# Kernel optimization log

Hardware: AMD Instinct MI355X
Metric: run time of the kernel (lower is better)

Reference implementation:

```python
import jax, jax.numpy as jnp
import numpy as np

B, D_IN, H, C = 8192, 256, 512, 10
EXPANSION = 2
INTER = int(H * EXPANSION * 2 / 3)  # 682, matches torch int(dim*expansion*2/3)
K_OUTER, H_CYCLES, L_CYCLES = 4, 2, 3
EPS = 1e-6


def rms_norm(x):
    return x * jax.lax.rsqrt(jnp.mean(x * x, axis=-1, keepdims=True) + EPS)


def swiglu(x, Wgu, Wd):
    gate, up = jnp.split(x @ Wgu, 2, axis=-1)
    return (jax.nn.silu(gate) * up) @ Wd


def setup_inputs() -> dict:
    key = jax.random.key(0)
    ks = jax.random.split(key, 13)
    s = 0.02
    return {
        "x": jax.random.normal(ks[0], (B, D_IN), jnp.float32),
        "W_in": jax.random.normal(ks[1], (D_IN, H), jnp.float32) * s,
        "b_in": jnp.zeros((H,), jnp.float32),
        "W_fb": jax.random.normal(ks[2], (C, H), jnp.float32) * s,
        "b_fb": jnp.zeros((H,), jnp.float32),
        "Wgu1": jax.random.normal(ks[3], (H, 2 * INTER), jnp.float32) * s,
        "Wd1": jax.random.normal(ks[4], (INTER, H), jnp.float32) * s,
        "Wgu2": jax.random.normal(ks[5], (H, 2 * INTER), jnp.float32) * s,
        "Wd2": jax.random.normal(ks[6], (INTER, H), jnp.float32) * s,
        "H_init": jax.random.normal(ks[7], (H,), jnp.float32) * s,
        "L_init": jax.random.normal(ks[8], (H,), jnp.float32) * s,
        "W_out": jax.random.normal(ks[9], (H, C), jnp.float32) * s,
        "b_out": jnp.zeros((C,), jnp.float32),
    }


def reference(x, W_in, b_in, W_fb, b_fb, Wgu1, Wd1, Wgu2, Wd2,
              H_init, L_init, W_out, b_out):
    def block(h):  # TRMBlock: two post-norm SwiGLU sublayers
        h = rms_norm(h + swiglu(h, Wgu1, Wd1))
        h = rms_norm(h + swiglu(h, Wgu2, Wd2))
        return h

    def level(hidden, injection):  # TRMLevel with n_layers=1
        return block(hidden + injection)

    x_proj = x @ W_in + b_in                       # [B,H]
    z_H = jnp.broadcast_to(H_init, (x.shape[0], H))
    z_L = jnp.broadcast_to(L_init, (x.shape[0], H))
    feedback = jnp.zeros((x.shape[0], H), x.dtype)
    all_logits = []
    for k in range(K_OUTER):
        combined = x_proj + feedback
        for _h in range(H_CYCLES):
            for _l in range(L_CYCLES):
                z_L = level(z_L, z_H + combined)
            z_H = level(z_H, z_L)
        if k < K_OUTER - 1:  # grad_last_only=True: no_grad + detach
            z_H = jax.lax.stop_gradient(z_H)
            z_L = jax.lax.stop_gradient(z_L)
        logits = z_H @ W_out + b_out               # [B,C]
        all_logits.append(logits)
        probs = jax.nn.softmax(jax.lax.stop_gradient(logits), axis=-1)
        feedback = probs @ W_fb + b_fb
    return logits, jnp.stack(all_logits)
```

## Files before the change

kernel.cpp:

```cpp
#include <hip/hip_runtime.h>

#define DEVI __device__ __forceinline__

typedef __attribute__((ext_vector_type(8)))  short short8;
typedef __attribute__((ext_vector_type(4)))  short short4v;
typedef __attribute__((ext_vector_type(16))) float f32x16;

constexpr int NROW = 8192;
constexpr int HD   = 512;
constexpr int DIN  = 256;
constexpr int NC   = 10;

constexpr int NP  = 22;
constexpr int KT1 = 32;
constexpr int KT2 = 44;
constexpr int KTX = 16;
constexpr int NTH = 16;

constexpr int KSTEP1 = NP*64*32;
constexpr int KSTEPD = NTH*64*16;

constexpr int SZ_P1  = (KT1+4)*KSTEP1;
constexpr int SZ_PD  = (KT2+4)*KSTEPD;
constexpr int SZ_PIN = (KTX+4)*KSTEPD;

DEVI short f2bf(float x){
  unsigned u = __builtin_bit_cast(unsigned, x);
  unsigned r = u + 0x7FFFu + ((u >> 16) & 1u);
  return (short)(r >> 16);
}
DEVI float bf2f(short s){
  unsigned u = ((unsigned)(unsigned short)s) << 16;
  return __builtin_bit_cast(float, u);
}
DEVI f32x16 MF(short8 a, short8 b, f32x16 c){
  return __builtin_amdgcn_mfma_f32_32x32x16_bf16(a, b, c, 0, 0, 0);
}
DEVI f32x16 fzero(){
  f32x16 v;
  #pragma unroll
  for (int i = 0; i < 16; ++i) v[i] = 0.f;
  return v;
}

DEVI void silu_store(int p, const f32x16& cg, const f32x16& cu,
                     short* INh_, short* INl_, int l)
{
  const int m = l & 31, g = l >> 5;
  #pragma unroll
  for (int q = 0; q < 4; ++q) {
    short4v hi, lo;
    #pragma unroll
    for (int pos = 0; pos < 4; ++pos) {
      const int r = q*4 + pos;
      float gv = cg[r], uv = cu[r];
      float sv = (gv / (1.0f + __expf(-gv))) * uv;
      short h = f2bf(sv);
      hi[pos] = h;
      lo[pos] = f2bf(sv - bf2f(h));
    }
    const int kt2  = 2*p + (q >> 1);
    const int slot = ((q & 1) << 5) + m;
    const int base = (kt2*64 + slot)*8 + (g << 2);
    *(short4v*)&INh_[base] = hi;
    *(short4v*)&INl_[base] = lo;
  }
}

DEVI void g1_pair(const short* __restrict__ bW,
                  const short* __restrict__ A1h_, const short* __restrict__ A1l_,
                  int l, f32x16& ag, f32x16& au)
{
  short8 R0[4], R1[4];
  auto LD = [&](short8* R, int kt) {
    const short* p = bW + (size_t)kt*KSTEP1;
    R[0] = *(const short8*)(p);
    R[1] = *(const short8*)(p + 8);
    R[2] = *(const short8*)(p + 16);
    R[3] = *(const short8*)(p + 24);
  };
  LD(R0, 0); LD(R1, 1);
  #pragma unroll 1
  for (int kt = 0; kt < KT1; kt += 2) {
    #define G1STEP(R, u) { \
      short8 bh = *(const short8*)&A1h_[((kt+u)*64 + l)*8]; \
      short8 bl = *(const short8*)&A1l_[((kt+u)*64 + l)*8]; \
      ag = MF(R[0], bh, ag); ag = MF(R[1], bh, ag); ag = MF(R[0], bl, ag); \
      au = MF(R[2], bh, au); au = MF(R[3], bh, au); au = MF(R[2], bl, au); \
      LD(R, kt + u + 2); }
    G1STEP(R0, 0) G1STEP(R1, 1)
    #undef G1STEP
  }
}

template<int KT>
DEVI void g2_run(const short* __restrict__ bD,
                 const short* __restrict__ Bh_, const short* __restrict__ Bl_,
                 int l, f32x16& c0, f32x16& c1)
{
  short8 R0[4], R1[4];
  auto LD = [&](short8* R, int kt) {
    const short* p = bD + (size_t)kt*KSTEPD;
    R[0] = *(const short8*)(p);
    R[1] = *(const short8*)(p + 8);
    R[2] = *(const short8*)(p + 1024);
    R[3] = *(const short8*)(p + 1032);
  };
  LD(R0, 0); LD(R1, 1);
  #pragma unroll 1
  for (int kt = 0; kt < KT; kt += 2) {
    #define G2STEP(R, u) { \
      short8 bh = *(const short8*)&Bh_[((kt+u)*64 + l)*8]; \
      short8 bl = *(const short8*)&Bl_[((kt+u)*64 + l)*8]; \
      c0 = MF(R[0], bh, c0); c0 = MF(R[1], bh, c0); c0 = MF(R[0], bl, c0); \
      c1 = MF(R[2], bh, c1); c1 = MF(R[3], bh, c1); c1 = MF(R[2], bl, c1); \
      LD(R, kt + u + 2); }
    G2STEP(R0, 0) G2STEP(R1, 1)
    #undef G2STEP
  }
}

DEVI void sublayer(float (&S)[32], const short* __restrict__ PW, const short* __restrict__ PD,
                   short* A1h_, short* A1l_, short* INh_, short* INl_,
                   float* rmsS_, int w, int l)
{
  const int m = l & 31, g = l >> 5;
  #pragma unroll
  for (int t = 0; t < 2; ++t) {
    #pragma unroll
    for (int q = 0; q < 4; ++q) {
      short4v hi, lo;
      #pragma unroll
      for (int pos = 0; pos < 4; ++pos) {
        float v = S[t*16 + q*4 + pos];
        short h = f2bf(v);
        hi[pos] = h;
        lo[pos] = f2bf(v - bf2f(h));
      }
      const int kt   = 4*w + 2*t + (q >> 1);
      const int slot = ((q & 1) << 5) + m;
      const int base = (kt*64 + slot)*8 + (g << 2);
      *(short4v*)&A1h_[base] = hi;
      *(short4v*)&A1l_[base] = lo;
    }
  }
  __syncthreads();
  {
    f32x16 ag = fzero(), au = fzero();
    g1_pair(PW + ((size_t)(w*64 + l))*32, A1h_, A1l_, l, ag, au);
    silu_store(w, ag, au, INh_, INl_, l);
  }
  {
    f32x16 ag = fzero(), au = fzero();
    g1_pair(PW + ((size_t)((w + 8)*64 + l))*32, A1h_, A1l_, l, ag, au);
    silu_store(w + 8, ag, au, INh_, INl_, l);
  }
  if (w < 6) {
    f32x16 ag = fzero(), au = fzero();
    g1_pair(PW + ((size_t)((w + 16)*64 + l))*32, A1h_, A1l_, l, ag, au);
    silu_store(w + 16, ag, au, INh_, INl_, l);
  }
  __syncthreads();
  f32x16 c0 = fzero(), c1 = fzero();
  g2_run<KT2>(PD + ((size_t)(2*w*64 + l))*16, INh_, INl_, l, c0, c1);
  float ss = 0.f;
  #pragma unroll
  for (int s = 0; s < 32; ++s) {
    float y = S[s] + (s < 16 ? c0[s & 15] : c1[s & 15]);
    S[s] = y;
    ss += y*y;
  }
  ss += __shfl_xor(ss, 32);
  if (l < 32) rmsS_[w*32 + l] = ss;
  __syncthreads();
  float tot = 0.f;
  #pragma unroll
  for (int wv = 0; wv < 8; ++wv) tot += rmsS_[wv*32 + m];
  const float rinv = 1.0f / sqrtf(tot * (1.0f/512.0f) + 1e-6f);
  #pragma unroll
  for (int s = 0; s < 32; ++s) S[s] *= rinv;
}

__global__
__attribute__((amdgpu_flat_work_group_size(512, 512)))
__attribute__((amdgpu_waves_per_eu(2, 2)))
void trm_main(
    const float* __restrict__ x,
    const float* __restrict__ b_in,
    const float* __restrict__ W_fb,
    const float* __restrict__ b_fb,
    const float* __restrict__ H_init,
    const float* __restrict__ L_init,
    const float* __restrict__ W_out,
    const float* __restrict__ b_out,
    float* __restrict__ xp,
    const short* __restrict__ PIN,
    const short* __restrict__ P1, const short* __restrict__ PD1,
    const short* __restrict__ P2, const short* __restrict__ PD2,
    float* __restrict__ out)
{
  __shared__ alignas(16) char smem[156672];
  short* A1h  = (short*)(smem);
  short* A1l  = (short*)(smem + 32768);
  short* INh  = (short*)(smem + 65536);
  short* INl  = (short*)(smem + 110592);
  float* rmsS = (float*)(smem + 155648);
  float* lgS  = (float*)(smem);
  float* pbS  = (float*)(smem + 10240);

  const int tid = threadIdx.x;
  const int l = tid & 63;
  const int w = tid >> 6;
  const int m = l & 31;
  const int g = l >> 5;
  const int wg = blockIdx.x;
  const int row0 = wg * 32;

  float zL[32], zH[32], cb[32];

  #pragma unroll
  for (int kk = 0; kk < 2; ++kk) {
    const int kt = 2*w + kk;
    const float4* xr = (const float4*)(x + (size_t)(row0 + m)*DIN + kt*16 + g*8);
    float4 v0 = xr[0];
    float4 v1 = xr[1];
    float v[8] = {v0.x, v0.y, v0.z, v0.w, v1.x, v1.y, v1.z, v1.w};
    short8 hi, lo;
    #pragma unroll
    for (int i = 0; i < 8; ++i) {
      short h = f2bf(v[i]);
      hi[i] = h;
      lo[i] = f2bf(v[i] - bf2f(h));
    }
    const int base = (kt*64 + l)*8;
    *(short8*)&A1h[base] = hi;
    *(short8*)&A1l[base] = lo;
  }
  __syncthreads();
  {
    f32x16 c0 = fzero(), c1 = fzero();
    g2_run<KTX>(PIN + ((size_t)(2*w*64 + l))*16, A1h, A1l, l, c0, c1);
    #pragma unroll
    for (int s = 0; s < 32; ++s) {
      const int r = s & 15;
      const int cc = w*64 + (s >> 4)*32 + (r & 3) + ((r >> 2) << 3) + (g << 2);
      float v = (s < 16 ? c0[r] : c1[r]) + b_in[cc];
      cb[s] = v;
      xp[(size_t)(wg*8 + w)*2048 + s*64 + l] = v;
      zH[s] = H_init[cc];
      zL[s] = L_init[cc];
    }
  }
  __syncthreads();

  #pragma unroll 1
  for (int k = 0; k < 4; ++k) {
    #pragma unroll 1
    for (int hc = 0; hc < 2; ++hc) {
      #pragma unroll 1
      for (int li = 0; li < 3; ++li) {
        #pragma unroll
        for (int s = 0; s < 32; ++s) zL[s] += zH[s] + cb[s];
        sublayer(zL, P1, PD1, A1h, A1l, INh, INl, rmsS, w, l);
        sublayer(zL, P2, PD2, A1h, A1l, INh, INl, rmsS, w, l);
      }
      #pragma unroll
      for (int s = 0; s < 32; ++s) zH[s] += zL[s];
      sublayer(zH, P1, PD1, A1h, A1l, INh, INl, rmsS, w, l);
      sublayer(zH, P2, PD2, A1h, A1l, INh, INl, rmsS, w, l);
    }
    {
      float part[10];
      #pragma unroll
      for (int c = 0; c < NC; ++c) part[c] = 0.f;
      #pragma unroll
      for (int s = 0; s < 32; ++s) {
        const int r = s & 15;
        const int cc = w*64 + (s >> 4)*32 + (r & 3) + ((r >> 2) << 3) + (g << 2);
        const float zz = zH[s];
        #pragma unroll
        for (int c = 0; c < NC; ++c) part[c] += zz * W_out[cc*NC + c];
      }
      #pragma unroll
      for (int c = 0; c < NC; ++c) part[c] += __shfl_xor(part[c], 32);
      if (l < 32) {
        #pragma unroll
        for (int c = 0; c < NC; ++c) lgS[(w*32 + l)*NC + c] = part[c];
      }
      __syncthreads();
      if (w == 0 && l < 32) {
        float lg[10];
        #pragma unroll
        for (int c = 0; c < NC; ++c) lg[c] = b_out[c];
        #pragma unroll
        for (int wv = 0; wv < 8; ++wv) {
          #pragma unroll
          for (int c = 0; c < NC; ++c) lg[c] += lgS[(wv*32 + l)*NC + c];
        }
        const int row = row0 + l;
        #pragma unroll
        for (int c = 0; c < NC; ++c) out[(size_t)(1 + k)*81920 + row*NC + c] = lg[c];
        if (k == 3) {
          #pragma unroll
          for (int c = 0; c < NC; ++c) out[row*NC + c] = lg[c];
        }
        float mx = lg[0];
        #pragma unroll
        for (int c = 1; c < NC; ++c) mx = fmaxf(mx, lg[c]);
        float e[10], sum = 0.f;
        #pragma unroll
        for (int c = 0; c < NC; ++c) { e[c] = __expf(lg[c] - mx); sum += e[c]; }
        const float inv = 1.0f / sum;
        #pragma unroll
        for (int c = 0; c < NC; ++c) pbS[l*NC + c] = e[c] * inv;
      }
      __syncthreads();
      if (k < 3) {
        #pragma unroll
        for (int s = 0; s < 32; ++s) {
          const int r = s & 15;
          const int cc = w*64 + (s >> 4)*32 + (r & 3) + ((r >> 2) << 3) + (g << 2);
          float fb = b_fb[cc];
          #pragma unroll
          for (int c = 0; c < NC; ++c) fb += pbS[m*NC + c] * W_fb[c*HD + cc];
          cb[s] = xp[(size_t)(wg*8 + w)*2048 + s*64 + l] + fb;
        }
      }
      __syncthreads();
    }
  }
}

__global__ void prep_gu(const float* __restrict__ Wgu, short* __restrict__ P)
{
  const int t = blockIdx.x*256 + threadIdx.x;
  if (t >= KT1*NP*64) return;
  const int l = t & 63;
  const int rest = t >> 6;
  const int nt = rest % NP;
  const int kt = rest / NP;
  const int n  = nt*32 + (l & 31);
  const int kb = kt*16 + (l >> 5)*8;
  short8 gh8, gl8, uh8, ul8;
  #pragma unroll
  for (int i = 0; i < 8; ++i) {
    float gv = 0.f, uv = 0.f;
    if (n < 682) {
      gv = Wgu[(size_t)(kb + i)*1364 + n];
      uv = Wgu[(size_t)(kb + i)*1364 + 682 + n];
    }
    short gh = f2bf(gv); gh8[i] = gh; gl8[i] = f2bf(gv - bf2f(gh));
    short uh = f2bf(uv); uh8[i] = uh; ul8[i] = f2bf(uv - bf2f(uh));
  }
  short* dst = P + ((size_t)(kt*NP + nt)*64 + l)*32;
  *(short8*)(dst)      = gh8;
  *(short8*)(dst + 8)  = gl8;
  *(short8*)(dst + 16) = uh8;
  *(short8*)(dst + 24) = ul8;
}

__global__ void prep_d(const float* __restrict__ Wd, short* __restrict__ P)
{
  const int t = blockIdx.x*256 + threadIdx.x;
  if (t >= KT2*NTH*64) return;
  const int l = t & 63;
  const int rest = t >> 6;
  const int nt = rest % NTH;
  const int kt2 = rest / NTH;
  const int n  = nt*32 + (l & 31);
  const int kb = kt2*16 + (l >> 5)*8;
  short8 h8, l8;
  #pragma unroll
  for (int i = 0; i < 8; ++i) {
    const int k2 = kb + i;
    float v = (k2 < 682) ? Wd[(size_t)k2*HD + n] : 0.f;
    short h = f2bf(v); h8[i] = h; l8[i] = f2bf(v - bf2f(h));
  }
  short* dst = P + ((size_t)(kt2*NTH + nt)*64 + l)*16;
  *(short8*)(dst)     = h8;
  *(short8*)(dst + 8) = l8;
}

__global__ void prep_in(const float* __restrict__ Win, short* __restrict__ P)
{
  const int t = blockIdx.x*256 + threadIdx.x;
  if (t >= KTX*NTH*64) return;
  const int l = t & 63;
  const int rest = t >> 6;
  const int nt = rest % NTH;
  const int kt = rest / NTH;
  const int n  = nt*32 + (l & 31);
  const int kb = kt*16 + (l >> 5)*8;
  short8 h8, l8;
  #pragma unroll
  for (int i = 0; i < 8; ++i) {
    float v = Win[(size_t)(kb + i)*HD + n];
    short h = f2bf(v); h8[i] = h; l8[i] = f2bf(v - bf2f(h));
  }
  short* dst = P + ((size_t)(kt*NTH + nt)*64 + l)*16;
  *(short8*)(dst)     = h8;
  *(short8*)(dst + 8) = l8;
}

extern "C" void kernel_launch(void* const* d_in, const int* in_sizes, int n_in,
                              void* d_out, int out_size, void* d_ws, size_t ws_size,
                              hipStream_t stream)
{
  const float* x     = (const float*)d_in[0];
  const float* W_in  = (const float*)d_in[1];
  const float* b_in  = (const float*)d_in[2];
  const float* W_fb  = (const float*)d_in[3];
  const float* b_fb  = (const float*)d_in[4];
  const float* Wgu1  = (const float*)d_in[5];
  const float* Wd1   = (const float*)d_in[6];
  const float* Wgu2  = (const float*)d_in[7];
  const float* Wd2   = (const float*)d_in[8];
  const float* Hini  = (const float*)d_in[9];
  const float* Lini  = (const float*)d_in[10];
  const float* W_out = (const float*)d_in[11];
  const float* b_out = (const float*)d_in[12];
  float* out = (float*)d_out;

  char* ws = (char*)d_ws;
  size_t off = 0;
  auto alloc = [&](size_t bytes) {
    char* p = ws + off;
    off = (off + bytes + 255) & ~(size_t)255;
    return p;
  };
  float* xp  = (float*)alloc((size_t)NROW*HD*4);
  short* PIN = (short*)alloc((size_t)SZ_PIN*2);
  short* P1  = (short*)alloc((size_t)SZ_P1*2);
  short* PD1 = (short*)alloc((size_t)SZ_PD*2);
  short* P2  = (short*)alloc((size_t)SZ_P1*2);
  short* PD2 = (short*)alloc((size_t)SZ_PD*2);

  const int n1 = KT1*NP*64;
  prep_gu<<<(n1+255)/256, 256, 0, stream>>>(Wgu1, P1);
  prep_gu<<<(n1+255)/256, 256, 0, stream>>>(Wgu2, P2);
  const int n2 = KT2*NTH*64;
  prep_d<<<(n2+255)/256, 256, 0, stream>>>(Wd1, PD1);
  prep_d<<<(n2+255)/256, 256, 0, stream>>>(Wd2, PD2);
  const int n3 = KTX*NTH*64;
  prep_in<<<(n3+255)/256, 256, 0, stream>>>(W_in, PIN);

  trm_main<<<256, 512, 0, stream>>>(x, b_in, W_fb, b_fb, Hini, Lini, W_out, b_out,
      xp, PIN, P1, PD1, P2, PD2, out);
}
```

Baseline: 4.937 ms.

## Spill combined injection to global and reload residual from LDS split-bf16

Moves the per-thread combined injection array (cb) out of registers into a global buffer reloaded with float4 reads inside each injecting sublayer. The injection add is fused into the bf16 hi/lo split, and the residual is rebuilt from the LDS hi+lo copy instead of being kept live in registers. The aim is to cut register pressure at two waves per EU and avoid spills. The cost is extra global traffic per sublayer. The residual is also rebuilt from a bf16x2 split rather than exact fp32, which may change precision slightly.

```diff
diff --git a/kernel.cpp b/kernel.cpp
--- a/kernel.cpp
+++ b/kernel.cpp
@@ -120,11 +120,22 @@
   }
 }
 
-DEVI void sublayer(float (&S)[32], const short* __restrict__ PW, const short* __restrict__ PD,
+template<int INJ>
+DEVI void sublayer(float (&S)[32], const float (&O)[32], const float* __restrict__ cbRow,
+                   const short* __restrict__ PW, const short* __restrict__ PD,
                    short* A1h_, short* A1l_, short* INh_, short* INl_,
                    float* rmsS_, int w, int l)
 {
   const int m = l & 31, g = l >> 5;
+  float inj[32];
+  if (INJ == 1) {
+    const float4* cbp = (const float4*)cbRow;
+    #pragma unroll
+    for (int i = 0; i < 8; ++i) {
+      float4 t4 = cbp[i];
+      inj[4*i+0] = t4.x; inj[4*i+1] = t4.y; inj[4*i+2] = t4.z; inj[4*i+3] = t4.w;
+    }
+  }
   #pragma unroll
   for (int t = 0; t < 2; ++t) {
     #pragma unroll
@@ -132,7 +143,10 @@
       short4v hi, lo;
       #pragma unroll
       for (int pos = 0; pos < 4; ++pos) {
-        float v = S[t*16 + q*4 + pos];
+        const int s = t*16 + q*4 + pos;
+        float v = S[s];
+        if (INJ == 1) v += O[s] + inj[s];
+        if (INJ == 2) v += O[s];
         short h = f2bf(v);
         hi[pos] = h;
         lo[pos] = f2bf(v - bf2f(h));
@@ -165,10 +179,23 @@
   g2_run<KT2>(PD + ((size_t)(2*w*64 + l))*16, INh_, INl_, l, c0, c1);
   float ss = 0.f;
   #pragma unroll
-  for (int s = 0; s < 32; ++s) {
-    float y = S[s] + (s < 16 ? c0[s & 15] : c1[s & 15]);
-    S[s] = y;
-    ss += y*y;
+  for (int t = 0; t < 2; ++t) {
+    #pragma unroll
+    for (int q = 0; q < 4; ++q) {
+      const int kt   = 4*w + 2*t + (q >> 1);
+      const int slot = ((q & 1) << 5) + m;
+      const int base = (kt*64 + slot)*8 + (g << 2);
+      short4v hi = *(const short4v*)&A1h_[base];
+      short4v lo = *(const short4v*)&A1l_[base];
+      #pragma unroll
+      for (int pos = 0; pos < 4; ++pos) {
+        const int s = t*16 + q*4 + pos;
+        float h0 = bf2f(hi[pos]) + bf2f(lo[pos]);
+        float y = h0 + (s < 16 ? c0[s & 15] : c1[s & 15]);
+        S[s] = y;
+        ss += y*y;
+      }
+    }
   }
   ss += __shfl_xor(ss, 32);
   if (l < 32) rmsS_[w*32 + l] = ss;
@@ -194,6 +221,7 @@
     const float* __restrict__ W_out,
     const float* __restrict__ b_out,
     float* __restrict__ xp,
+    float* __restrict__ cbG,
     const short* __restrict__ PIN,
     const short* __restrict__ P1, const short* __restrict__ PD1,
     const short* __restrict__ P2, const short* __restrict__ PD2,
@@ -216,7 +244,9 @@
   const int wg = blockIdx.x;
   const int row0 = wg * 32;
 
-  float zL[32], zH[32], cb[32];
+  float zL[32], zH[32];
+  const size_t rowbase = (size_t)(wg*8 + w)*2048 + l*32;
+  const float* cbRow = cbG + rowbase;
 
   #pragma unroll
   for (int kk = 0; kk < 2; ++kk) {
@@ -240,15 +270,23 @@
   {
     f32x16 c0 = fzero(), c1 = fzero();
     g2_run<KTX>(PIN + ((size_t)(2*w*64 + l))*16, A1h, A1l, l, c0, c1);
+    float vals[32];
     #pragma unroll
     for (int s = 0; s < 32; ++s) {
       const int r = s & 15;
       const int cc = w*64 + (s >> 4)*32 + (r & 3) + ((r >> 2) << 3) + (g << 2);
       float v = (s < 16 ? c0[r] : c1[r]) + b_in[cc];
-      cb[s] = v;
-      xp[(size_t)(wg*8 + w)*2048 + s*64 + l] = v;
+      vals[s] = v;
       zH[s] = H_init[cc];
       zL[s] = L_init[cc];
+    }
+    float4* xpw = (float4*)(xp + rowbase);
+    float4* cbw = (float4*)(cbG + rowbase);
+    #pragma unroll
+    for (int i = 0; i < 8; ++i) {
+      float4 t4 = { vals[4*i+0], vals[4*i+1], vals[4*i+2], vals[4*i+3] };
+      xpw[i] = t4;
+      cbw[i] = t4;
     }
   }
   __syncthreads();
@@ -259,15 +297,11 @@
     for (int hc = 0; hc < 2; ++hc) {
       #pragma unroll 1
       for (int li = 0; li < 3; ++li) {
-        #pragma unroll
-        for (int s = 0; s < 32; ++s) zL[s] += zH[s] + cb[s];
-        sublayer(zL, P1, PD1, A1h, A1l, INh, INl, rmsS, w, l);
-        sublayer(zL, P2, PD2, A1h, A1l, INh, INl, rmsS, w, l);
-      }
-      #pragma unroll
-      for (int s = 0; s < 32; ++s) zH[s] += zL[s];
-      sublayer(zH, P1, PD1, A1h, A1l, INh, INl, rmsS, w, l);
-      sublayer(zH, P2, PD2, A1h, A1l, INh, INl, rmsS, w, l);
+        sublayer<1>(zL, zH, cbRow, P1, PD1, A1h, A1l, INh, INl, rmsS, w, l);
+        sublayer<0>(zL, zH, cbRow, P2, PD2, A1h, A1l, INh, INl, rmsS, w, l);
+      }
+      sublayer<2>(zH, zL, cbRow, P1, PD1, A1h, A1l, INh, INl, rmsS, w, l);
+      sublayer<0>(zH, zL, cbRow, P2, PD2, A1h, A1l, INh, INl, rmsS, w, l);
     }
     {
       float part[10];
@@ -316,14 +350,33 @@
       }
       __syncthreads();
       if (k < 3) {
+        float pb[10];
+        #pragma unroll
+        for (int c = 0; c < NC; ++c) pb[c] = pbS[m*NC + c];
+        float xa[32];
+        {
+          const float4* xpr = (const float4*)(xp + rowbase);
+          #pragma unroll
+          for (int i = 0; i < 8; ++i) {
+            float4 t4 = xpr[i];
+            xa[4*i+0] = t4.x; xa[4*i+1] = t4.y; xa[4*i+2] = t4.z; xa[4*i+3] = t4.w;
+          }
+        }
+        float cbv[32];
         #pragma unroll
         for (int s = 0; s < 32; ++s) {
           const int r = s & 15;
           const int cc = w*64 + (s >> 4)*32 + (r & 3) + ((r >> 2) << 3) + (g << 2);
           float fb = b_fb[cc];
           #pragma unroll
-          for (int c = 0; c < NC; ++c) fb += pbS[m*NC + c] * W_fb[c*HD + cc];
-          cb[s] = xp[(size_t)(wg*8 + w)*2048 + s*64 + l] + fb;
+          for (int c = 0; c < NC; ++c) fb += pb[c] * W_fb[c*HD + cc];
+          cbv[s] = xa[s] + fb;
+        }
+        float4* cbw = (float4*)(cbG + rowbase);
+        #pragma unroll
+        for (int i = 0; i < 8; ++i) {
+          float4 t4 = { cbv[4*i+0], cbv[4*i+1], cbv[4*i+2], cbv[4*i+3] };
+          cbw[i] = t4;
         }
       }
       __syncthreads();
@@ -429,6 +482,7 @@
     return p;
   };
   float* xp  = (float*)alloc((size_t)NROW*HD*4);
+  float* cbG = (float*)alloc((size_t)NROW*HD*4);
   short* PIN = (short*)alloc((size_t)SZ_PIN*2);
   short* P1  = (short*)alloc((size_t)SZ_P1*2);
   short* PD1 = (short*)alloc((size_t)SZ_PD*2);
@@ -445,5 +499,5 @@
   prep_in<<<(n3+255)/256, 256, 0, stream>>>(W_in, PIN);
 
   trm_main<<<256, 512, 0, stream>>>(x, b_in, W_fb, b_fb, Hini, Lini, W_out, b_out,
-      xp, PIN, P1, PD1, P2, PD2, out);
-}
+      xp, cbG, PIN, P1, PD1, P2, PD2, out);
+}
```

Result: slower. 5.042 ms (+2.1%).
